# Kernel optimization log

Measured on AMD Instinct MI355X. Metric: run time of the kernel, lower is better.

## Reference

```python
import jax, jax.numpy as jnp
import numpy as np

PAD_IDX = 0


def setup_inputs() -> dict:
    key = jax.random.key(0)
    ks = jax.random.split(key, 6)
    nentries, entry_size, bsize, nemb, vocab = 8000, 32, 64, 256, 50000
    keys = jax.random.randint(ks[0], (nentries,), 0, vocab)
    entries = jax.random.randint(ks[1], (nentries, entry_size), 0, vocab)
    query = jax.random.normal(ks[2], (bsize, nemb), dtype=jnp.float32)
    wordemb = jax.random.normal(ks[3], (vocab, nemb), dtype=jnp.float32)
    qproj_w = jax.random.uniform(ks[4], (nemb, nemb), jnp.float32, -0.1, 0.1)
    qproj_b = jnp.zeros((nemb,), jnp.float32)
    return dict(keys=keys, entries=entries, query=query, wordemb=wordemb,
                qproj_w=qproj_w, qproj_b=qproj_b)


def _embed(ids, wordemb):
    # F.embedding with padding_idx: gathered rows at pad_idx are zeroed
    return wordemb[ids] * (ids != PAD_IDX)[..., None].astype(wordemb.dtype)


def reference(keys, entries, query, wordemb, qproj_w, qproj_b):
    keys_e = _embed(keys, wordemb)       # (m, d)
    ents_e = _embed(entries, wordemb)    # (m, n, d)
    # --- single hop (max_hops = 1) ---
    # value_atten: query attends over the n tokens inside each entry
    vq = query @ qproj_w.T + qproj_b                       # (b, d)
    logits_v = jnp.einsum('ik,mnk->imn', vq, ents_e)       # (b, m, n)
    prob_v = jax.nn.softmax(logits_v, axis=-1)
    ents = jnp.einsum('imn,mnk->imk', prob_v, ents_e)      # (b, m, d)
    # entry_atten: query attends over entries via their keys
    logits_e = jnp.einsum('ik,jk->ij', query, keys_e)      # (b, m)
    prob_e = jax.nn.softmax(logits_e, axis=-1)
    o_k = prob_e @ keys_e                                  # (b, d)
    combined = jnp.einsum('bm,bme->be', prob_e, ents)      # (b, d)
    # return (us[-1], prob_list[-1], combined_entries)
    return o_k, logits_e, combined
```

## Files before the change

kernel.cpp:

```cpp
#include <hip/hip_runtime.h>
#include <math.h>

#define B 64
#define D 256
#define M 8000
#define N 32
#define LG_LD 8000
#define EPB 16
#define NBLK (M / EPB)

typedef unsigned short u16;
typedef __bf16 bf16x8 __attribute__((ext_vector_type(8)));
typedef float fx4 __attribute__((ext_vector_type(4)));

#define STR_E  264
#define STR_P  40

static __device__ __forceinline__ u16 f2bf(float x) {
    unsigned int u = __float_as_uint(x);
    u += 0x7FFFu + ((u >> 16) & 1u);
    return (u16)(u >> 16);
}
static __device__ __forceinline__ float bf2f(u16 h) {
    return __uint_as_float(((unsigned)h) << 16);
}

__global__ __launch_bounds__(256) void k_prep(const int* __restrict__ keys,
                                              const float* __restrict__ emb,
                                              const float* __restrict__ q,
                                              const float* __restrict__ W,
                                              const float* __restrict__ bias,
                                              u16* __restrict__ embb,
                                              u16* __restrict__ qbf,
                                              u16* __restrict__ keb,
                                              u16* __restrict__ vqb) {
    __shared__ float qs[D];
    int t = threadIdx.x, bid = blockIdx.x;
    if (bid < 6250) {
        size_t idx = (size_t)bid * 2048 + (size_t)t * 8;
        float4 v0 = *(const float4*)(emb + idx);
        float4 v1 = *(const float4*)(emb + idx + 4);
        u16 h[8] = {f2bf(v0.x), f2bf(v0.y), f2bf(v0.z), f2bf(v0.w),
                    f2bf(v1.x), f2bf(v1.y), f2bf(v1.z), f2bf(v1.w)};
        *(uint4*)(embb + idx) = *(uint4*)h;
    } else if (bid < 6258) {
        size_t idx = (size_t)(bid - 6250) * 2048 + (size_t)t * 8;
        float4 v0 = *(const float4*)(q + idx);
        float4 v1 = *(const float4*)(q + idx + 4);
        u16 h[8] = {f2bf(v0.x), f2bf(v0.y), f2bf(v0.z), f2bf(v0.w),
                    f2bf(v1.x), f2bf(v1.y), f2bf(v1.z), f2bf(v1.w)};
        *(uint4*)(qbf + idx) = *(uint4*)h;
    } else if (bid < 7258) {
        int c = (bid - 6258) * 256 + t;
        int j = c >> 5, sp = c & 31;
        int id = keys[j];
        const float* rp = emb + (size_t)id * D + sp * 8;
        float4 v0 = *(const float4*)rp;
        float4 v1 = *(const float4*)(rp + 4);
        float msk = (id != 0) ? 1.f : 0.f;
        u16 h[8] = {f2bf(v0.x * msk), f2bf(v0.y * msk), f2bf(v0.z * msk), f2bf(v0.w * msk),
                    f2bf(v1.x * msk), f2bf(v1.y * msk), f2bf(v1.z * msk), f2bf(v1.w * msk)};
        *(uint4*)(keb + (size_t)j * D + sp * 8) = *(uint4*)h;
    } else {
        int b = bid - 7258;
        qs[t] = q[b * D + t];
        __syncthreads();
        const float* wr = W + t * D;
        float acc = bias[t];
#pragma unroll 8
        for (int k = 0; k < D; k += 4) {
            float4 w4 = *(const float4*)(wr + k);
            acc += qs[k] * w4.x + qs[k + 1] * w4.y + qs[k + 2] * w4.z + qs[k + 3] * w4.w;
        }
        vqb[b * D + t] = f2bf(acc);
    }
}

__global__ __launch_bounds__(256) void k_logits_f(const u16* __restrict__ qbf,
                                                  const u16* __restrict__ keb,
                                                  float* __restrict__ lg,
                                                  float* __restrict__ lgT) {
    int t = threadIdx.x;
    int lane = t & 63, l = lane & 15, q = lane >> 4, w = t >> 6;
    int m0 = blockIdx.x * 16;
    int b0 = 16 * w;
    fx4 acc = {0.f, 0.f, 0.f, 0.f};
#pragma unroll
    for (int s = 0; s < 8; ++s) {
        bf16x8 a  = *(const bf16x8*)(qbf + (size_t)(b0 + l) * D + 32 * s + 8 * q);
        bf16x8 bb = *(const bf16x8*)(keb + (size_t)(m0 + l) * D + 32 * s + 8 * q);
        acc = __builtin_amdgcn_mfma_f32_16x16x32_bf16(a, bb, acc, 0, 0, 0);
    }
#pragma unroll
    for (int r = 0; r < 4; ++r) {
        lg[(size_t)(b0 + 4 * q + r) * LG_LD + m0 + l] = acc[r];
        lgT[(size_t)(m0 + l) * B + b0 + 4 * q + r] = acc[r];
    }
}

__global__ __launch_bounds__(256, 2) void k_heavy_f(const int* __restrict__ entries,
                                                    const u16* __restrict__ embb,
                                                    const u16* __restrict__ vqb,
                                                    const u16* __restrict__ keb,
                                                    const float* __restrict__ lgT,
                                                    u16* __restrict__ numCp,
                                                    u16* __restrict__ numKp,
                                                    float* __restrict__ mLp,
                                                    float* __restrict__ denLp) {
    __shared__ __align__(16) u16 sEu[2][N * STR_E];
    __shared__ __align__(16) u16 sETu[2][64 * 136];
    __shared__ __align__(16) u16 sPu[B * STR_P];
    __shared__ float sw[EPB][B];
    __shared__ float red[4][B];

    int t = threadIdx.x;
    int lane = t & 63, l = lane & 15, q = lane >> 4, w = t >> 6;
    int b0 = 16 * w;
    int sp = t & 31, n0 = t >> 5;
    int m0 = blockIdx.x * EPB;
    int bb = t & 63, y = t >> 6;

    float lv[4];
#pragma unroll
    for (int i = 0; i < 4; ++i) lv[i] = lgT[(size_t)(m0 + 4 * i + y) * B + bb];
    float mx4 = fmaxf(fmaxf(lv[0], lv[1]), fmaxf(lv[2], lv[3]));
    red[y][bb] = mx4;
    __syncthreads();
    float mL = fmaxf(fmaxf(red[0][bb], red[1][bb]), fmaxf(red[2][bb], red[3][bb]));
    __syncthreads();
    float ds = 0.f;
#pragma unroll
    for (int i = 0; i < 4; ++i) {
        float wv = __expf(lv[i] - mL);
        sw[4 * i + y][bb] = wv;
        ds += wv;
    }
    red[y][bb] = ds;
    bf16x8 vqf[8];
#pragma unroll
    for (int s = 0; s < 8; ++s)
        vqf[s] = *(const bf16x8*)(vqb + (b0 + l) * D + 32 * s + 8 * q);
    __syncthreads();
    if (t < B) {
        mLp[blockIdx.x * B + t] = mL;
        denLp[blockIdx.x * B + t] = red[0][t] + red[1][t] + red[2][t] + red[3][t];
    }

    fx4 zero4 = {0.f, 0.f, 0.f, 0.f};
    fx4 acc[16];
#pragma unroll
    for (int dt = 0; dt < 16; ++dt) acc[dt] = zero4;

    int idc[4], idn[4];
    uint4 pf[4];
#pragma unroll
    for (int i = 0; i < 4; ++i) idc[i] = entries[m0 * N + n0 + 8 * i];
#pragma unroll
    for (int i = 0; i < 4; ++i)
        pf[i] = *(const uint4*)(embb + (size_t)idc[i] * D + sp * 8);
#pragma unroll
    for (int i = 0; i < 4; ++i) {
        if (idc[i] == 0) pf[i] = make_uint4(0u, 0u, 0u, 0u);
        *(uint4*)&sEu[0][(n0 + 8 * i) * STR_E + sp * 8] = pf[i];
    }
#pragma unroll
    for (int j = 0; j < 8; ++j) {
        unsigned a0 = (((unsigned*)&pf[0])[j >> 1] >> ((j & 1) * 16)) & 0xFFFFu;
        unsigned a1 = (((unsigned*)&pf[1])[j >> 1] >> ((j & 1) * 16)) & 0xFFFFu;
        unsigned a2 = (((unsigned*)&pf[2])[j >> 1] >> ((j & 1) * 16)) & 0xFFFFu;
        unsigned a3 = (((unsigned*)&pf[3])[j >> 1] >> ((j & 1) * 16)) & 0xFFFFu;
        uint2 pr = make_uint2(a0 | (a1 << 16), a2 | (a3 << 16));
        int off = (2 * sp + (j >> 2)) * 136 + (n0 >> 1) * 32 + (j & 3) * 8 + (n0 & 1) * 4;
        *(uint2*)&sETu[0][off] = pr;
    }
#pragma unroll
    for (int i = 0; i < 4; ++i) idc[i] = entries[(m0 + 1) * N + n0 + 8 * i];
#pragma unroll
    for (int i = 0; i < 4; ++i)
        pf[i] = *(const uint4*)(embb + (size_t)idc[i] * D + sp * 8);
#pragma unroll
    for (int i = 0; i < 4; ++i) idn[i] = entries[(m0 + 2) * N + n0 + 8 * i];

    int offL = (l >> 2) * 136 + (l & 3) * 8;

#pragma unroll 2
    for (int e = 0; e < EPB; ++e) {
        __syncthreads();
        int nxt = (e + 1) & 1;
        if (e < EPB - 1) {
#pragma unroll
            for (int i = 0; i < 4; ++i) {
                if (idc[i] == 0) pf[i] = make_uint4(0u, 0u, 0u, 0u);
                *(uint4*)&sEu[nxt][(n0 + 8 * i) * STR_E + sp * 8] = pf[i];
            }
#pragma unroll
            for (int j = 0; j < 8; ++j) {
                unsigned a0 = (((unsigned*)&pf[0])[j >> 1] >> ((j & 1) * 16)) & 0xFFFFu;
                unsigned a1 = (((unsigned*)&pf[1])[j >> 1] >> ((j & 1) * 16)) & 0xFFFFu;
                unsigned a2 = (((unsigned*)&pf[2])[j >> 1] >> ((j & 1) * 16)) & 0xFFFFu;
                unsigned a3 = (((unsigned*)&pf[3])[j >> 1] >> ((j & 1) * 16)) & 0xFFFFu;
                uint2 pr = make_uint2(a0 | (a1 << 16), a2 | (a3 << 16));
                int off = (2 * sp + (j >> 2)) * 136 + (n0 >> 1) * 32 + (j & 3) * 8 + (n0 & 1) * 4;
                *(uint2*)&sETu[nxt][off] = pr;
            }
            if (e < EPB - 2) {
#pragma unroll
                for (int i = 0; i < 4; ++i)
                    pf[i] = *(const uint4*)(embb + (size_t)idn[i] * D + sp * 8);
#pragma unroll
                for (int i = 0; i < 4; ++i) idc[i] = idn[i];
                if (e < EPB - 3) {
#pragma unroll
                    for (int i = 0; i < 4; ++i) idn[i] = entries[(m0 + e + 3) * N + n0 + 8 * i];
                }
            }
        }
        int cur = e & 1;
        fx4 accS[2];
        accS[0] = zero4; accS[1] = zero4;
#pragma unroll
        for (int T = 0; T < 2; ++T)
#pragma unroll
            for (int s = 0; s < 8; ++s) {
                bf16x8 ea = *(const bf16x8*)&sEu[cur][(16 * T + l) * STR_E + 32 * s + 8 * q];
                accS[T] = __builtin_amdgcn_mfma_f32_16x16x32_bf16(ea, vqf[s], accS[T], 0, 0, 0);
            }
        float swb = sw[e][b0 + l];
        float mx = -INFINITY;
#pragma unroll
        for (int T = 0; T < 2; ++T)
#pragma unroll
            for (int r = 0; r < 4; ++r) mx = fmaxf(mx, accS[T][r]);
        mx = fmaxf(mx, __shfl_xor(mx, 16));
        mx = fmaxf(mx, __shfl_xor(mx, 32));
        float pe[2][4], sum = 0.f;
#pragma unroll
        for (int T = 0; T < 2; ++T)
#pragma unroll
            for (int r = 0; r < 4; ++r) {
                pe[T][r] = __expf(accS[T][r] - mx);
                sum += pe[T][r];
            }
        sum += __shfl_xor(sum, 16);
        sum += __shfl_xor(sum, 32);
        float sc = swb / sum;
#pragma unroll
        for (int T = 0; T < 2; ++T)
#pragma unroll
            for (int r = 0; r < 4; ++r) {
                int nn = 16 * T + 4 * q + r;
                int slot = 4 * (nn & 7) + (nn >> 3);
                sPu[(b0 + l) * STR_P + slot] = f2bf(pe[T][r] * sc);
            }
        bf16x8 pa = *(const bf16x8*)&sPu[(b0 + l) * STR_P + 8 * q];
#pragma unroll
        for (int dt = 0; dt < 16; ++dt) {
            bf16x8 eb = *(const bf16x8*)&sETu[cur][offL + dt * 544 + q * 32];
            acc[dt] = __builtin_amdgcn_mfma_f32_16x16x32_bf16(pa, eb, acc[dt], 0, 0, 0);
        }
    }

    u16* ncp = numCp + (size_t)blockIdx.x * (B * D);
#pragma unroll
    for (int dt = 0; dt < 16; ++dt)
#pragma unroll
        for (int r = 0; r < 4; ++r)
            ncp[(b0 + 4 * q + r) * D + 16 * dt + l] = f2bf(acc[dt][r]);

    __syncthreads();
    {
        int rp = t >> 5;
        uint4 ka = *(const uint4*)(keb + (size_t)(m0 + rp) * D + sp * 8);
        uint4 kb = *(const uint4*)(keb + (size_t)(m0 + rp + 8) * D + sp * 8);
#pragma unroll
        for (int j = 0; j < 8; ++j) {
            unsigned a0 = (((unsigned*)&ka)[j >> 1] >> ((j & 1) * 16)) & 0xFFFFu;
            unsigned a1 = (((unsigned*)&kb)[j >> 1] >> ((j & 1) * 16)) & 0xFFFFu;
            int d = 8 * sp + j;
            int sl = 2 * rp;
            int off = (d >> 2) * 136 + (sl >> 3) * 32 + (d & 3) * 8 + (sl & 7);
            *(unsigned*)&sETu[0][off] = a0 | (a1 << 16);
        }
#pragma unroll
        for (int i = 0; i < 4; ++i) {
            int m = 4 * i + y;
            int slot = 2 * (m & 7) + (m >> 3);
            sPu[bb * STR_P + slot] = f2bf(sw[m][bb]);
        }
        *(uint2*)&sPu[bb * STR_P + 16 + 4 * y] = make_uint2(0u, 0u);
    }
    __syncthreads();
    fx4 acc2[16];
#pragma unroll
    for (int dt = 0; dt < 16; ++dt) acc2[dt] = zero4;
    {
        bf16x8 pa2 = *(const bf16x8*)&sPu[(b0 + l) * STR_P + 8 * q];
#pragma unroll
        for (int dt = 0; dt < 16; ++dt) {
            bf16x8 eb2 = *(const bf16x8*)&sETu[0][offL + dt * 544 + q * 32];
            acc2[dt] = __builtin_amdgcn_mfma_f32_16x16x32_bf16(pa2, eb2, acc2[dt], 0, 0, 0);
        }
    }
    u16* nkp = numKp + (size_t)blockIdx.x * (B * D);
#pragma unroll
    for (int dt = 0; dt < 16; ++dt)
#pragma unroll
        for (int r = 0; r < 4; ++r)
            nkp[(b0 + 4 * q + r) * D + 16 * dt + l] = f2bf(acc2[dt][r]);
}

__global__ __launch_bounds__(128) void k_gstat(const float* __restrict__ mLp,
                                               const float* __restrict__ denLp,
                                               float* __restrict__ Mg,
                                               float* __restrict__ rden) {
    __shared__ float red[128];
    int b = blockIdx.x, t = threadIdx.x;
    float mx = -INFINITY;
    for (int blk = t; blk < NBLK; blk += 128) mx = fmaxf(mx, mLp[blk * B + b]);
    red[t] = mx;
    __syncthreads();
    for (int s = 64; s > 0; s >>= 1) {
        if (t < s) red[t] = fmaxf(red[t], red[t + s]);
        __syncthreads();
    }
    float mg = red[0];
    __syncthreads();
    float ds = 0.f;
    for (int blk = t; blk < NBLK; blk += 128)
        ds += __expf(mLp[blk * B + b] - mg) * denLp[blk * B + b];
    red[t] = ds;
    __syncthreads();
    for (int s = 64; s > 0; s >>= 1) {
        if (t < s) red[t] += red[t + s];
        __syncthreads();
    }
    if (t == 0) { Mg[b] = mg; rden[b] = 1.f / red[0]; }
}

__global__ __launch_bounds__(256) void k_comb2(const u16* __restrict__ numCp,
                                               const u16* __restrict__ numKp,
                                               const float* __restrict__ mLp,
                                               const float* __restrict__ Mg,
                                               const float* __restrict__ rden,
                                               float* __restrict__ o_k,
                                               float* __restrict__ comb) {
    __shared__ float ro[8][32], rc[8][32];
    int bid = blockIdx.x;
    int b = bid >> 3, d0 = (bid & 7) * 32;
    int t = threadIdx.x;
    int dd = t & 31, s = t >> 5;
    float mg = Mg[b];
    float ao = 0.f, ac = 0.f;
    for (int blk = s; blk < NBLK; blk += 8) {
        float sc = __expf(mLp[blk * B + b] - mg);
        size_t i = (size_t)blk * (B * D) + (size_t)b * D + d0 + dd;
        ao += sc * bf2f(numKp[i]);
        ac += sc * bf2f(numCp[i]);
    }
    ro[s][dd] = ao;
    rc[s][dd] = ac;
    __syncthreads();
    if (t < 32) {
        float so = 0.f, sc2 = 0.f;
#pragma unroll
        for (int k = 0; k < 8; ++k) { so += ro[k][t]; sc2 += rc[k][t]; }
        float rd = rden[b];
        o_k[b * D + d0 + t] = so * rd;
        comb[b * D + d0 + t] = sc2 * rd;
    }
}


extern "C" void kernel_launch(void* const* d_in, const int* in_sizes, int n_in,
                              void* d_out, int out_size, void* d_ws, size_t ws_size,
                              hipStream_t stream) {
    const int*   keys    = (const int*)d_in[0];
    const int*   entries = (const int*)d_in[1];
    const float* query   = (const float*)d_in[2];
    const float* wordemb = (const float*)d_in[3];
    const float* qproj_w = (const float*)d_in[4];
    const float* qproj_b = (const float*)d_in[5];

    float* out  = (float*)d_out;
    float* o_k  = out;
    float* lg   = out + B * D;
    float* comb = out + B * D + B * M;

    char* wsb = (char*)d_ws;
    u16*   embb  = (u16*)wsb;
    u16*   keb   = (u16*)(wsb + 25600000);
    u16*   qbf   = (u16*)(wsb + 29696000);
    u16*   vqb   = (u16*)(wsb + 29728768);
    float* lgT   = (float*)(wsb + 29761536);
    u16*   numCp = (u16*)(wsb + 31809536);
    u16*   numKp = (u16*)(wsb + 48193536);
    float* mLp   = (float*)(wsb + 64577536);
    float* denLp = (float*)(wsb + 64705536);
    float* Mg    = (float*)(wsb + 64833536);
    float* rden  = (float*)(wsb + 64833792);

    k_prep<<<7322, 256, 0, stream>>>(keys, wordemb, query, qproj_w, qproj_b,
                                     embb, qbf, keb, vqb);
    k_logits_f<<<NBLK, 256, 0, stream>>>(qbf, keb, lg, lgT);
    k_heavy_f<<<NBLK, 256, 0, stream>>>(entries, embb, vqb, keb, lgT,
                                        numCp, numKp, mLp, denLp);
    k_gstat<<<B, 128, 0, stream>>>(mLp, denLp, Mg, rden);
    k_comb2<<<512, 256, 0, stream>>>(numCp, numKp, mLp, Mg, rden, o_k, comb);
}
```

Measured before the change: 188.9 us.

## Fuse entry logits into heavy kernel and global stats into combine kernel

Result: faster. 184.9 us (-2.1%).

```diff
diff --git a/kernel.cpp b/kernel.cpp
--- a/kernel.cpp
+++ b/kernel.cpp
@@ -76,33 +76,12 @@
     }
 }
 
-__global__ __launch_bounds__(256) void k_logits_f(const u16* __restrict__ qbf,
-                                                  const u16* __restrict__ keb,
-                                                  float* __restrict__ lg,
-                                                  float* __restrict__ lgT) {
-    int t = threadIdx.x;
-    int lane = t & 63, l = lane & 15, q = lane >> 4, w = t >> 6;
-    int m0 = blockIdx.x * 16;
-    int b0 = 16 * w;
-    fx4 acc = {0.f, 0.f, 0.f, 0.f};
-#pragma unroll
-    for (int s = 0; s < 8; ++s) {
-        bf16x8 a  = *(const bf16x8*)(qbf + (size_t)(b0 + l) * D + 32 * s + 8 * q);
-        bf16x8 bb = *(const bf16x8*)(keb + (size_t)(m0 + l) * D + 32 * s + 8 * q);
-        acc = __builtin_amdgcn_mfma_f32_16x16x32_bf16(a, bb, acc, 0, 0, 0);
-    }
-#pragma unroll
-    for (int r = 0; r < 4; ++r) {
-        lg[(size_t)(b0 + 4 * q + r) * LG_LD + m0 + l] = acc[r];
-        lgT[(size_t)(m0 + l) * B + b0 + 4 * q + r] = acc[r];
-    }
-}
-
 __global__ __launch_bounds__(256, 2) void k_heavy_f(const int* __restrict__ entries,
                                                     const u16* __restrict__ embb,
                                                     const u16* __restrict__ vqb,
+                                                    const u16* __restrict__ qbf,
                                                     const u16* __restrict__ keb,
-                                                    const float* __restrict__ lgT,
+                                                    float* __restrict__ lg,
                                                     u16* __restrict__ numCp,
                                                     u16* __restrict__ numKp,
                                                     float* __restrict__ mLp,
@@ -111,7 +90,6 @@
     __shared__ __align__(16) u16 sETu[2][64 * 136];
     __shared__ __align__(16) u16 sPu[B * STR_P];
     __shared__ float sw[EPB][B];
-    __shared__ float red[4][B];
 
     int t = threadIdx.x;
     int lane = t & 63, l = lane & 15, q = lane >> 4, w = t >> 6;
@@ -120,44 +98,55 @@
     int m0 = blockIdx.x * EPB;
     int bb = t & 63, y = t >> 6;
 
-    float lv[4];
-#pragma unroll
-    for (int i = 0; i < 4; ++i) lv[i] = lgT[(size_t)(m0 + 4 * i + y) * B + bb];
-    float mx4 = fmaxf(fmaxf(lv[0], lv[1]), fmaxf(lv[2], lv[3]));
-    red[y][bb] = mx4;
-    __syncthreads();
-    float mL = fmaxf(fmaxf(red[0][bb], red[1][bb]), fmaxf(red[2][bb], red[3][bb]));
-    __syncthreads();
-    float ds = 0.f;
-#pragma unroll
-    for (int i = 0; i < 4; ++i) {
-        float wv = __expf(lv[i] - mL);
-        sw[4 * i + y][bb] = wv;
-        ds += wv;
-    }
-    red[y][bb] = ds;
+    int idc[4], idn[4];
+    uint4 pf[4];
+#pragma unroll
+    for (int i = 0; i < 4; ++i) idc[i] = entries[m0 * N + n0 + 8 * i];
+#pragma unroll
+    for (int i = 0; i < 4; ++i)
+        pf[i] = *(const uint4*)(embb + (size_t)idc[i] * D + sp * 8);
+
+    fx4 zero4 = {0.f, 0.f, 0.f, 0.f};
+    fx4 aL = zero4;
+#pragma unroll
+    for (int s = 0; s < 8; ++s) {
+        bf16x8 a  = *(const bf16x8*)(qbf + (size_t)(b0 + l) * D + 32 * s + 8 * q);
+        bf16x8 bq = *(const bf16x8*)(keb + (size_t)(m0 + l) * D + 32 * s + 8 * q);
+        aL = __builtin_amdgcn_mfma_f32_16x16x32_bf16(a, bq, aL, 0, 0, 0);
+    }
+#pragma unroll
+    for (int r = 0; r < 4; ++r)
+        lg[(size_t)(b0 + 4 * q + r) * LG_LD + m0 + l] = aL[r];
+
+#pragma unroll
+    for (int r = 0; r < 4; ++r) {
+        float m_ = aL[r];
+        m_ = fmaxf(m_, __shfl_xor(m_, 1));
+        m_ = fmaxf(m_, __shfl_xor(m_, 2));
+        m_ = fmaxf(m_, __shfl_xor(m_, 4));
+        m_ = fmaxf(m_, __shfl_xor(m_, 8));
+        float wv = __expf(aL[r] - m_);
+        sw[l][b0 + 4 * q + r] = wv;
+        float d_ = wv;
+        d_ += __shfl_xor(d_, 1);
+        d_ += __shfl_xor(d_, 2);
+        d_ += __shfl_xor(d_, 4);
+        d_ += __shfl_xor(d_, 8);
+        if (l == 0) {
+            mLp[blockIdx.x * B + b0 + 4 * q + r] = m_;
+            denLp[blockIdx.x * B + b0 + 4 * q + r] = d_;
+        }
+    }
+
     bf16x8 vqf[8];
 #pragma unroll
     for (int s = 0; s < 8; ++s)
         vqf[s] = *(const bf16x8*)(vqb + (b0 + l) * D + 32 * s + 8 * q);
-    __syncthreads();
-    if (t < B) {
-        mLp[blockIdx.x * B + t] = mL;
-        denLp[blockIdx.x * B + t] = red[0][t] + red[1][t] + red[2][t] + red[3][t];
-    }
-
-    fx4 zero4 = {0.f, 0.f, 0.f, 0.f};
+
     fx4 acc[16];
 #pragma unroll
     for (int dt = 0; dt < 16; ++dt) acc[dt] = zero4;
 
-    int idc[4], idn[4];
-    uint4 pf[4];
-#pragma unroll
-    for (int i = 0; i < 4; ++i) idc[i] = entries[m0 * N + n0 + 8 * i];
-#pragma unroll
-    for (int i = 0; i < 4; ++i)
-        pf[i] = *(const uint4*)(embb + (size_t)idc[i] * D + sp * 8);
 #pragma unroll
     for (int i = 0; i < 4; ++i) {
         if (idc[i] == 0) pf[i] = make_uint4(0u, 0u, 0u, 0u);
@@ -309,50 +298,47 @@
             nkp[(b0 + 4 * q + r) * D + 16 * dt + l] = f2bf(acc2[dt][r]);
 }
 
-__global__ __launch_bounds__(128) void k_gstat(const float* __restrict__ mLp,
-                                               const float* __restrict__ denLp,
-                                               float* __restrict__ Mg,
-                                               float* __restrict__ rden) {
-    __shared__ float red[128];
-    int b = blockIdx.x, t = threadIdx.x;
-    float mx = -INFINITY;
-    for (int blk = t; blk < NBLK; blk += 128) mx = fmaxf(mx, mLp[blk * B + b]);
-    red[t] = mx;
-    __syncthreads();
-    for (int s = 64; s > 0; s >>= 1) {
-        if (t < s) red[t] = fmaxf(red[t], red[t + s]);
-        __syncthreads();
-    }
-    float mg = red[0];
-    __syncthreads();
-    float ds = 0.f;
-    for (int blk = t; blk < NBLK; blk += 128)
-        ds += __expf(mLp[blk * B + b] - mg) * denLp[blk * B + b];
-    red[t] = ds;
-    __syncthreads();
-    for (int s = 64; s > 0; s >>= 1) {
-        if (t < s) red[t] += red[t + s];
-        __syncthreads();
-    }
-    if (t == 0) { Mg[b] = mg; rden[b] = 1.f / red[0]; }
-}
-
 __global__ __launch_bounds__(256) void k_comb2(const u16* __restrict__ numCp,
                                                const u16* __restrict__ numKp,
                                                const float* __restrict__ mLp,
-                                               const float* __restrict__ Mg,
-                                               const float* __restrict__ rden,
+                                               const float* __restrict__ denLp,
                                                float* __restrict__ o_k,
                                                float* __restrict__ comb) {
+    __shared__ float sscale[NBLK];
+    __shared__ float red[256];
     __shared__ float ro[8][32], rc[8][32];
+    __shared__ float srden;
     int bid = blockIdx.x;
     int b = bid >> 3, d0 = (bid & 7) * 32;
     int t = threadIdx.x;
+    float mx = -INFINITY;
+    for (int blk = t; blk < NBLK; blk += 256) mx = fmaxf(mx, mLp[blk * B + b]);
+    red[t] = mx;
+    __syncthreads();
+    for (int s = 128; s > 0; s >>= 1) {
+        if (t < s) red[t] = fmaxf(red[t], red[t + s]);
+        __syncthreads();
+    }
+    float Mg = red[0];
+    __syncthreads();
+    float ds = 0.f;
+    for (int blk = t; blk < NBLK; blk += 256) {
+        float sc = __expf(mLp[blk * B + b] - Mg);
+        sscale[blk] = sc;
+        ds += sc * denLp[blk * B + b];
+    }
+    red[t] = ds;
+    __syncthreads();
+    for (int s = 128; s > 0; s >>= 1) {
+        if (t < s) red[t] += red[t + s];
+        __syncthreads();
+    }
+    if (t == 0) srden = 1.f / red[0];
+    __syncthreads();
     int dd = t & 31, s = t >> 5;
-    float mg = Mg[b];
     float ao = 0.f, ac = 0.f;
     for (int blk = s; blk < NBLK; blk += 8) {
-        float sc = __expf(mLp[blk * B + b] - mg);
+        float sc = sscale[blk];
         size_t i = (size_t)blk * (B * D) + (size_t)b * D + d0 + dd;
         ao += sc * bf2f(numKp[i]);
         ac += sc * bf2f(numCp[i]);
@@ -364,7 +350,7 @@
         float so = 0.f, sc2 = 0.f;
 #pragma unroll
         for (int k = 0; k < 8; ++k) { so += ro[k][t]; sc2 += rc[k][t]; }
-        float rd = rden[b];
+        float rd = srden;
         o_k[b * D + d0 + t] = so * rd;
         comb[b * D + d0 + t] = sc2 * rd;
     }
@@ -391,19 +377,14 @@
     u16*   keb   = (u16*)(wsb + 25600000);
     u16*   qbf   = (u16*)(wsb + 29696000);
     u16*   vqb   = (u16*)(wsb + 29728768);
-    float* lgT   = (float*)(wsb + 29761536);
-    u16*   numCp = (u16*)(wsb + 31809536);
-    u16*   numKp = (u16*)(wsb + 48193536);
-    float* mLp   = (float*)(wsb + 64577536);
-    float* denLp = (float*)(wsb + 64705536);
-    float* Mg    = (float*)(wsb + 64833536);
-    float* rden  = (float*)(wsb + 64833792);
+    u16*   numCp = (u16*)(wsb + 29761536);
+    u16*   numKp = (u16*)(wsb + 46145536);
+    float* mLp   = (float*)(wsb + 62529536);
+    float* denLp = (float*)(wsb + 62657536);
 
     k_prep<<<7322, 256, 0, stream>>>(keys, wordemb, query, qproj_w, qproj_b,
                                      embb, qbf, keb, vqb);
-    k_logits_f<<<NBLK, 256, 0, stream>>>(qbf, keb, lg, lgT);
-    k_heavy_f<<<NBLK, 256, 0, stream>>>(entries, embb, vqb, keb, lgT,
+    k_heavy_f<<<NBLK, 256, 0, stream>>>(entries, embb, vqb, qbf, keb, lg,
                                         numCp, numKp, mLp, denLp);
-    k_gstat<<<B, 128, 0, stream>>>(mLp, denLp, Mg, rden);
-    k_comb2<<<512, 256, 0, stream>>>(numCp, numKp, mLp, Mg, rden, o_k, comb);
-}
+    k_comb2<<<512, 256, 0, stream>>>(numCp, numKp, mLp, denLp, o_k, comb);
+}
```
